# Kernel optimization log

Measured on AMD Instinct MI355X. Metric: run time of the kernel, lower is better.

The kernel has to match this reference:

```python
import jax, jax.numpy as jnp
import numpy as np

D = 2048   # dec_hidden_size == enc_hidden_size
IN = 512   # input_size
T = 4096   # T_enc


def setup_inputs() -> dict:
    key = jax.random.key(0)
    ks = jax.random.split(key, 20)
    s = 0.02
    zeros = jnp.zeros
    return {
        "data": jax.random.normal(ks[0], (1, IN), jnp.float32),
        "h0": jax.random.normal(ks[1], (1, 1, D), jnp.float32),
        "c0": jax.random.normal(ks[2], (1, 1, D), jnp.float32),
        "enc_output": jax.random.normal(ks[3], (T, 1, D), jnp.float32),
        "pi": jax.random.normal(ks[4], (T,), jnp.float32),
        "W_w": jax.random.normal(ks[5], (D, D), jnp.float32) * s,
        "U_w": jax.random.normal(ks[6], (D, D), jnp.float32) * s,
        "V_w": jax.random.normal(ks[7], (1, D), jnp.float32) * s,
        "lin_w": jax.random.normal(ks[8], (D, D), jnp.float32) * s,
        "lin_b": zeros((D,), jnp.float32),
        "lin1_w": jax.random.normal(ks[9], (D, D), jnp.float32) * s,
        "lin1_b": zeros((D,), jnp.float32),
        "lin2_w": jax.random.normal(ks[10], (D, D), jnp.float32) * s,
        "lin2_b": zeros((D,), jnp.float32),
        "dense_w": jax.random.normal(ks[11], (1, D), jnp.float32) * s,
        "dense_b": zeros((1,), jnp.float32),
        "W_ih": jax.random.normal(ks[12], (4 * D, IN + D), jnp.float32) * s,
        "W_hh": jax.random.normal(ks[13], (4 * D, D), jnp.float32) * s,
        "b_ih": zeros((4 * D,), jnp.float32),
        "b_hh": zeros((4 * D,), jnp.float32),
        "i": 100,
    }


def reference(data, h0, c0, enc_output, pi, W_w, U_w, V_w, lin_w, lin_b,
              lin1_w, lin1_b, lin2_w, lin2_b, dense_w, dense_b,
              W_ih, W_hh, b_ih, b_hh, i):
    Tl = pi.shape[0]
    output_pos = i + 1
    enc = enc_output[:, 0, :]                      # (T, E)
    # binary_vector(output_pos, T) @ pi : row k gets pi[output_pos+T-k-2] iff k >= output_pos-1
    k = jnp.arange(Tl)
    idx = output_pos + Tl - k - 2
    prod = jnp.where(k >= output_pos - 1, pi[jnp.clip(idx, 0, Tl - 1)], 0.0)
    u_h = (enc @ U_w.T) * prod[:, None]            # (T, D), per-channel scale by prod
    q = h0[0, 0] @ W_w.T                           # (D,)
    score = jnp.tanh(q[None, :] + u_h) @ V_w[0]    # (T,)
    score = jnp.where(k < output_pos, 0.0, score)  # attn_score[:j_null] = 0 (zero, not -inf)
    attn = jax.nn.softmax(score)                   # softmax over T
    context = attn @ enc                           # (E,)
    x = jnp.concatenate([context, data[0]])        # (E + IN,)
    # single-step LSTM, PyTorch gate order i,f,g,o
    gates = x @ W_ih.T + b_ih + h0[0, 0] @ W_hh.T + b_hh
    gi, gf, gg, go = jnp.split(gates, 4)
    c_new = jax.nn.sigmoid(gf) * c0[0, 0] + jax.nn.sigmoid(gi) * jnp.tanh(gg)
    h_new = jax.nn.sigmoid(go) * jnp.tanh(c_new)
    fc = h_new @ lin_w.T + lin_b
    l1 = fc @ lin1_w.T + lin1_b
    delta = jax.nn.softmax(l1)
    beta = jax.nn.softplus(fc @ lin2_w.T + lin2_b)
    gamma = l1 @ dense_w.T + dense_b               # original reuses linear1 for lin3
    return (gamma, beta, delta, h_new, c_new)
```

## Files before the change

### kernel.cpp

```cpp
#include <hip/hip_runtime.h>
#include <hip/hip_bf16.h>

#define D_  2048
#define IN_ 512
#define T_  4096
#define G4_ 8192

typedef __attribute__((ext_vector_type(4))) float f32x4;
typedef __attribute__((ext_vector_type(8))) short s16x8;
typedef unsigned short u16;

#define WS_PROD    0
#define WS_Q       (T_)
#define WS_X       (T_ + D_)
#define WS_PARTIAL (WS_X + D_ + IN_)
#define WS_ATTN    (WS_PARTIAL + T_*16)
#define WS_GATES   (WS_ATTN + T_)
#define WS_G2      (WS_GATES + G4_)
#define WS_FC      (WS_G2 + G4_)
#define WS_L1      (WS_FC + D_)
#define WS_HN      (WS_L1 + D_)
#define WS_BF16    (WS_HN + D_)
#define WS_FAST_BYTES ((size_t)WS_BF16 * 4 + ((size_t)T_ * D_ + (size_t)D_ * D_) * 2)

typedef const __attribute__((address_space(1))) void gas_t;
typedef __attribute__((address_space(3))) void las_t;

__device__ inline u16 bfbits(float f) {
  union { __hip_bfloat16 b; u16 s; } u; u.b = __float2bfloat16(f); return u.s;
}
__device__ inline float bf2f(u16 s) {
  union { unsigned u; float f; } v; v.u = ((unsigned)s) << 16; return v.f;
}

__device__ inline float wave_dot4(const float* __restrict__ w,
                                  const float* __restrict__ x, int n4, int lane) {
  float s = 0.f;
  const f32x4* w4 = (const f32x4*)w;
  const f32x4* x4 = (const f32x4*)x;
  for (int c = lane; c < n4; c += 64) {
    f32x4 a = w4[c], b = x4[c];
    s += a[0]*b[0] + a[1]*b[1] + a[2]*b[2] + a[3]*b[3];
  }
  #pragma unroll
  for (int m = 32; m >= 1; m >>= 1) s += __shfl_xor(s, m, 64);
  return s;
}

__global__ __launch_bounds__(256) void k_convert(const float* __restrict__ Ww,
    const float* __restrict__ h0, const float* __restrict__ pi,
    const float* __restrict__ data, const int* __restrict__ ip,
    const float* __restrict__ enc, const float* __restrict__ Uw,
    int do_convert, float* __restrict__ ws) {
  const int gidx = blockIdx.x * 256 + threadIdx.x;
  const int nth = 1024 * 256;
  if (do_convert) {
    u16* encB = (u16*)(ws + WS_BF16);
    u16* UwB  = encB + (size_t)T_ * D_;
    for (int c = gidx; c < (T_ * D_) / 8; c += nth) {
      const size_t base = (size_t)c * 8;
      f32x4 v0 = *(const f32x4*)(enc + base);
      f32x4 v1 = *(const f32x4*)(enc + base + 4);
      u16 t[8];
      #pragma unroll
      for (int e = 0; e < 4; ++e) { t[e] = bfbits(v0[e]); t[4 + e] = bfbits(v1[e]); }
      *(s16x8*)&encB[base] = *(s16x8*)&t[0];
    }
    for (int c = gidx; c < (D_ * D_) / 8; c += nth) {
      const size_t base = (size_t)c * 8;
      f32x4 v0 = *(const f32x4*)(Uw + base);
      f32x4 v1 = *(const f32x4*)(Uw + base + 4);
      u16 t[8];
      #pragma unroll
      for (int e = 0; e < 4; ++e) { t[e] = bfbits(v0[e]); t[4 + e] = bfbits(v1[e]); }
      *(s16x8*)&UwB[base] = *(s16x8*)&t[0];
    }
  }
  const int op = ip[0] + 1;
  if (gidx < T_) {
    float p = 0.f;
    if (gidx >= op - 1) {
      int idx = op + T_ - gidx - 2;
      idx = idx < 0 ? 0 : (idx > T_ - 1 ? T_ - 1 : idx);
      p = pi[idx];
    }
    ws[WS_PROD + gidx] = p;
  }
  if (gidx < D_) ws[WS_X + gidx] = 0.f;
  if (gidx < IN_) ws[WS_X + D_ + gidx] = data[gidx];
  const int gw = gidx >> 6, lane = gidx & 63;
  if (gw < D_) {
    float s = wave_dot4(Ww + (size_t)gw * D_, h0, D_ / 4, lane);
    if (lane == 0) ws[WS_Q + gw] = s;
  }
}

__global__ __launch_bounds__(512, 4) void k_gemm_bf16(
    const float* __restrict__ Vw, const float* __restrict__ h0,
    const float* __restrict__ Whh, float* __restrict__ ws) {
  __shared__ __align__(16) u16 Ah[128 * 64];
  __shared__ __align__(16) u16 Bh[128 * 64];
  const u16* encB = (const u16*)(ws + WS_BF16);
  const u16* UwB  = encB + (size_t)T_ * D_;
  const int tid = threadIdx.x, lane = tid & 63, wid = tid >> 6;
  const int wr = wid >> 2, wc = wid & 3;
  const int g = lane >> 4, lr = lane & 15;
  const int bid = blockIdx.x;
  const int wgid = (bid & 7) * 64 + (bid >> 3);
  const int mb = wgid >> 4, nb = wgid & 15;

  f32x4 acc[4][2];
  #pragma unroll
  for (int m = 0; m < 4; ++m)
    #pragma unroll
    for (int n = 0; n < 2; ++n) acc[m][n] = (f32x4){0.f, 0.f, 0.f, 0.f};

  const int c0 = tid,        r0 = c0 >> 3, s0 = (c0 & 7) ^ (r0 & 7);
  const int c1 = tid + 512,  r1 = c1 >> 3, s1 = (c1 & 7) ^ (r1 & 7);
  const u16* ga0 = encB + (size_t)(mb * 128 + r0) * D_ + s0 * 8;
  const u16* ga1 = encB + (size_t)(mb * 128 + r1) * D_ + s1 * 8;
  const u16* gb0 = UwB  + (size_t)(nb * 128 + r0) * D_ + s0 * 8;
  const u16* gb1 = UwB  + (size_t)(nb * 128 + r1) * D_ + s1 * 8;
  u16* la0 = &Ah[c0 * 8]; u16* la1 = &Ah[c1 * 8];
  u16* lb0 = &Bh[c0 * 8]; u16* lb1 = &Bh[c1 * 8];

  for (int ks = 0; ks < D_ / 64; ++ks) {
    __syncthreads();
    __builtin_amdgcn_global_load_lds((gas_t*)(ga0 + ks * 64), (las_t*)la0, 16, 0, 0);
    __builtin_amdgcn_global_load_lds((gas_t*)(ga1 + ks * 64), (las_t*)la1, 16, 0, 0);
    __builtin_amdgcn_global_load_lds((gas_t*)(gb0 + ks * 64), (las_t*)lb0, 16, 0, 0);
    __builtin_amdgcn_global_load_lds((gas_t*)(gb1 + ks * 64), (las_t*)lb1, 16, 0, 0);
    __syncthreads();
    #pragma unroll
    for (int kk = 0; kk < 2; ++kk) {
      const int koff = kk * 64 + g * 16;
      s16x8 af[4], bf[2];
      #pragma unroll
      for (int m = 0; m < 4; ++m) {
        const int r = wr * 64 + m * 16 + lr;
        af[m] = *(const s16x8*)((const char*)Ah + r * 128 + (koff ^ ((r & 7) << 4)));
      }
      #pragma unroll
      for (int n = 0; n < 2; ++n) {
        const int r = wc * 32 + n * 16 + lr;
        bf[n] = *(const s16x8*)((const char*)Bh + r * 128 + (koff ^ ((r & 7) << 4)));
      }
      #pragma unroll
      for (int m = 0; m < 4; ++m)
        #pragma unroll
        for (int n = 0; n < 2; ++n)
          acc[m][n] = __builtin_amdgcn_mfma_f32_16x16x32_bf16(af[m], bf[n], acc[m][n], 0, 0, 0);
    }
  }

  const float* q    = ws + WS_Q;
  const float* prod = ws + WS_PROD;
  float Vv[2], qv[2];
  #pragma unroll
  for (int n = 0; n < 2; ++n) {
    const int d = nb * 128 + wc * 32 + n * 16 + lr;
    Vv[n] = Vw[d]; qv[n] = q[d];
  }
  __syncthreads();
  float* red = (float*)Ah;
  #pragma unroll
  for (int m = 0; m < 4; ++m) {
    #pragma unroll
    for (int r = 0; r < 4; ++r) {
      const int t_loc = wr * 64 + m * 16 + g * 4 + r;
      const float p = prod[mb * 128 + t_loc];
      float s = Vv[0] * tanhf(qv[0] + p * acc[m][0][r])
              + Vv[1] * tanhf(qv[1] + p * acc[m][1][r]);
      s += __shfl_xor(s, 1, 64);
      s += __shfl_xor(s, 2, 64);
      s += __shfl_xor(s, 4, 64);
      s += __shfl_xor(s, 8, 64);
      if (lr == 0) red[t_loc * 4 + wc] = s;
    }
  }
  __syncthreads();
  if (tid < 128) {
    const float s = red[tid * 4] + red[tid * 4 + 1] + red[tid * 4 + 2] + red[tid * 4 + 3];
    ws[WS_PARTIAL + (size_t)(mb * 128 + tid) * 16 + nb] = s;
  }

  const int rbase = bid * 16 + wid * 2;
  #pragma unroll
  for (int rr = 0; rr < 2; ++rr) {
    const int row = rbase + rr;
    float s = wave_dot4(Whh + (size_t)row * D_, h0, D_ / 4, lane);
    if (lane == 0) ws[WS_G2 + row] = s;
  }
}

__global__ __launch_bounds__(512, 4) void k_gemm_f32(
    const float* __restrict__ enc, const float* __restrict__ Uw,
    const float* __restrict__ Vw, const float* __restrict__ h0,
    const float* __restrict__ Whh, float* __restrict__ ws) {
  __shared__ __align__(16) u16 sbuf[2 * 128 * 40];
  u16* Ah = sbuf;
  u16* Bh = sbuf + 128 * 40;
  const int tid = threadIdx.x;
  const int lane = tid & 63, wid = tid >> 6;
  const int wr = wid >> 2, wc = wid & 3;
  const int g = lane >> 4, lr = lane & 15;
  const int mb = blockIdx.x, nb = blockIdx.y;

  f32x4 acc[4][2];
  #pragma unroll
  for (int m = 0; m < 4; ++m)
    #pragma unroll
    for (int n = 0; n < 2; ++n) acc[m][n] = (f32x4){0.f, 0.f, 0.f, 0.f};

  const int srow = tid >> 2;
  const int scol = (tid & 3) * 8;
  const float* pa0 = enc + (size_t)(mb * 128 + srow) * D_ + scol;
  const float* pb0 = Uw  + (size_t)(nb * 128 + srow) * D_ + scol;
  const int sidx = srow * 40 + scol;

  f32x4 an0 = *(const f32x4*)(pa0);
  f32x4 an1 = *(const f32x4*)(pa0 + 4);
  f32x4 bn0 = *(const f32x4*)(pb0);
  f32x4 bn1 = *(const f32x4*)(pb0 + 4);

  for (int ks = 0; ks < 64; ++ks) {
    f32x4 a0 = an0, a1 = an1, b0 = bn0, b1 = bn1;
    if (ks < 63) {
      an0 = *(const f32x4*)(pa0 + (ks + 1) * 32);
      an1 = *(const f32x4*)(pa0 + (ks + 1) * 32 + 4);
      bn0 = *(const f32x4*)(pb0 + (ks + 1) * 32);
      bn1 = *(const f32x4*)(pb0 + (ks + 1) * 32 + 4);
    }
    __syncthreads();
    __align__(16) u16 ah[8], bh[8];
    #pragma unroll
    for (int e = 0; e < 4; ++e) {
      ah[e] = bfbits(a0[e]); ah[4 + e] = bfbits(a1[e]);
      bh[e] = bfbits(b0[e]); bh[4 + e] = bfbits(b1[e]);
    }
    *(s16x8*)&Ah[sidx] = *(s16x8*)&ah[0];
    *(s16x8*)&Bh[sidx] = *(s16x8*)&bh[0];
    __syncthreads();

    s16x8 af[4], bf[2];
    #pragma unroll
    for (int m = 0; m < 4; ++m)
      af[m] = *(const s16x8*)&Ah[(wr * 64 + m * 16 + lr) * 40 + g * 8];
    #pragma unroll
    for (int n = 0; n < 2; ++n)
      bf[n] = *(const s16x8*)&Bh[(wc * 32 + n * 16 + lr) * 40 + g * 8];
    #pragma unroll
    for (int m = 0; m < 4; ++m)
      #pragma unroll
      for (int n = 0; n < 2; ++n)
        acc[m][n] = __builtin_amdgcn_mfma_f32_16x16x32_bf16(af[m], bf[n], acc[m][n], 0, 0, 0);
  }

  const float* q    = ws + WS_Q;
  const float* prod = ws + WS_PROD;
  float Vv[2], qv[2];
  #pragma unroll
  for (int n = 0; n < 2; ++n) {
    const int d = nb * 128 + wc * 32 + n * 16 + lr;
    Vv[n] = Vw[d]; qv[n] = q[d];
  }
  __syncthreads();
  float* red = (float*)sbuf;
  #pragma unroll
  for (int m = 0; m < 4; ++m) {
    #pragma unroll
    for (int r = 0; r < 4; ++r) {
      const int t_loc = wr * 64 + m * 16 + g * 4 + r;
      const float p = prod[mb * 128 + t_loc];
      float s = Vv[0] * tanhf(qv[0] + p * acc[m][0][r])
              + Vv[1] * tanhf(qv[1] + p * acc[m][1][r]);
      s += __shfl_xor(s, 1, 64);
      s += __shfl_xor(s, 2, 64);
      s += __shfl_xor(s, 4, 64);
      s += __shfl_xor(s, 8, 64);
      if (lr == 0) red[t_loc * 4 + wc] = s;
    }
  }
  __syncthreads();
  if (tid < 128) {
    const float s = red[tid * 4] + red[tid * 4 + 1] + red[tid * 4 + 2] + red[tid * 4 + 3];
    ws[WS_PARTIAL + (size_t)(mb * 128 + tid) * 16 + nb] = s;
  }
  const int flat = blockIdx.y * gridDim.x + blockIdx.x;
  const int rbase = flat * 16 + wid * 2;
  #pragma unroll
  for (int rr = 0; rr < 2; ++rr) {
    const int row = rbase + rr;
    float s = wave_dot4(Whh + (size_t)row * D_, h0, D_ / 4, lane);
    if (lane == 0) ws[WS_G2 + row] = s;
  }
}

__global__ __launch_bounds__(1024) void k_attn(const int* __restrict__ ip,
                                               float* __restrict__ ws) {
  __shared__ float sm[16];
  const int tid = threadIdx.x, lane = tid & 63, wid = tid >> 6;
  const int op = ip[0] + 1;
  float v[4];
  #pragma unroll
  for (int j = 0; j < 4; ++j) {
    const int t = tid + j * 1024;
    const f32x4* p = (const f32x4*)(ws + WS_PARTIAL + (size_t)t * 16);
    f32x4 p0 = p[0], p1 = p[1], p2 = p[2], p3 = p[3];
    float s = (p0[0]+p0[1]+p0[2]+p0[3]) + (p1[0]+p1[1]+p1[2]+p1[3])
            + (p2[0]+p2[1]+p2[2]+p2[3]) + (p3[0]+p3[1]+p3[2]+p3[3]);
    v[j] = (t < op) ? 0.f : s;
  }
  float mx = fmaxf(fmaxf(v[0], v[1]), fmaxf(v[2], v[3]));
  #pragma unroll
  for (int m = 32; m >= 1; m >>= 1) mx = fmaxf(mx, __shfl_xor(mx, m, 64));
  if (lane == 0) sm[wid] = mx;
  __syncthreads();
  if (tid == 0) {
    float m2 = sm[0];
    for (int w = 1; w < 16; ++w) m2 = fmaxf(m2, sm[w]);
    sm[0] = m2;
  }
  __syncthreads();
  mx = sm[0];
  __syncthreads();
  float e[4], ls = 0.f;
  #pragma unroll
  for (int j = 0; j < 4; ++j) { e[j] = expf(v[j] - mx); ls += e[j]; }
  #pragma unroll
  for (int m = 32; m >= 1; m >>= 1) ls += __shfl_xor(ls, m, 64);
  if (lane == 0) sm[wid] = ls;
  __syncthreads();
  if (tid == 0) {
    float s2 = 0.f;
    for (int w = 0; w < 16; ++w) s2 += sm[w];
    sm[0] = s2;
  }
  __syncthreads();
  const float inv = 1.f / sm[0];
  #pragma unroll
  for (int j = 0; j < 4; ++j) ws[WS_ATTN + tid + j * 1024] = e[j] * inv;
}

__global__ __launch_bounds__(256) void k_context_bf16(float* __restrict__ ws) {
  const u16* encB = (const u16*)(ws + WS_BF16);
  const int d = blockIdx.x * 256 + threadIdx.x;
  const int t0 = blockIdx.y * 256;
  const float* attn = ws + WS_ATTN;
  float s = 0.f;
  for (int t = t0; t < t0 + 256; ++t) s += attn[t] * bf2f(encB[(size_t)t * D_ + d]);
  atomicAdd(&ws[WS_X + d], s);
}
__global__ __launch_bounds__(256) void k_context_f32(const float* __restrict__ enc,
                                                     float* __restrict__ ws) {
  const int d = blockIdx.x * 256 + threadIdx.x;
  const int t0 = blockIdx.y * 256;
  const float* attn = ws + WS_ATTN;
  float s = 0.f;
  for (int t = t0; t < t0 + 256; ++t) s += attn[t] * enc[(size_t)t * D_ + d];
  atomicAdd(&ws[WS_X + d], s);
}

__global__ __launch_bounds__(256) void k_gatecell(const float* __restrict__ Wih,
    const float* __restrict__ bih, const float* __restrict__ bhh,
    const float* __restrict__ c0, float* __restrict__ ws, float* __restrict__ out) {
  const int wid = threadIdx.x >> 6, lane = threadIdx.x & 63;
  const int d = blockIdx.x * 4 + wid;
  const f32x4* x4 = (const f32x4*)(ws + WS_X);
  const f32x4* r0 = (const f32x4*)(Wih + (size_t)(0 * D_ + d) * (D_ + IN_));
  const f32x4* r1 = (const f32x4*)(Wih + (size_t)(1 * D_ + d) * (D_ + IN_));
  const f32x4* r2 = (const f32x4*)(Wih + (size_t)(2 * D_ + d) * (D_ + IN_));
  const f32x4* r3 = (const f32x4*)(Wih + (size_t)(3 * D_ + d) * (D_ + IN_));
  float s0 = 0.f, s1 = 0.f, s2 = 0.f, s3 = 0.f;
  for (int c = lane; c < (D_ + IN_) / 4; c += 64) {
    f32x4 x = x4[c];
    f32x4 a0 = r0[c], a1 = r1[c], a2 = r2[c], a3 = r3[c];
    s0 += a0[0]*x[0] + a0[1]*x[1] + a0[2]*x[2] + a0[3]*x[3];
    s1 += a1[0]*x[0] + a1[1]*x[1] + a1[2]*x[2] + a1[3]*x[3];
    s2 += a2[0]*x[0] + a2[1]*x[1] + a2[2]*x[2] + a2[3]*x[3];
    s3 += a3[0]*x[0] + a3[1]*x[1] + a3[2]*x[2] + a3[3]*x[3];
  }
  #pragma unroll
  for (int m = 32; m >= 1; m >>= 1) {
    s0 += __shfl_xor(s0, m, 64);
    s1 += __shfl_xor(s1, m, 64);
    s2 += __shfl_xor(s2, m, 64);
    s3 += __shfl_xor(s3, m, 64);
  }
  if (lane == 0) {
    const float gi = s0 + ws[WS_G2 + 0 * D_ + d] + bih[0 * D_ + d] + bhh[0 * D_ + d];
    const float gf = s1 + ws[WS_G2 + 1 * D_ + d] + bih[1 * D_ + d] + bhh[1 * D_ + d];
    const float gg = s2 + ws[WS_G2 + 2 * D_ + d] + bih[2 * D_ + d] + bhh[2 * D_ + d];
    const float go = s3 + ws[WS_G2 + 3 * D_ + d] + bih[3 * D_ + d] + bhh[3 * D_ + d];
    const float si = 1.f / (1.f + expf(-gi));
    const float sf = 1.f / (1.f + expf(-gf));
    const float so = 1.f / (1.f + expf(-go));
    const float cn = sf * c0[d] + si * tanhf(gg);
    const float hn = so * tanhf(cn);
    out[1 + 2 * D_ + d] = hn;
    out[1 + 3 * D_ + d] = cn;
    ws[WS_HN + d] = hn;
  }
}

__global__ __launch_bounds__(256) void k_fc(const float* __restrict__ lw,
    const float* __restrict__ lb, float* __restrict__ ws) {
  const int wid = threadIdx.x >> 6, lane = threadIdx.x & 63;
  const int row = blockIdx.x * 4 + wid;
  float s = wave_dot4(lw + (size_t)row * D_, ws + WS_HN, D_ / 4, lane);
  if (lane == 0) ws[WS_FC + row] = s + lb[row];
}

__global__ __launch_bounds__(256) void k_l1beta(const float* __restrict__ l1w,
    const float* __restrict__ l1b, const float* __restrict__ l2w,
    const float* __restrict__ l2b, float* __restrict__ ws, float* __restrict__ out) {
  const int wid = threadIdx.x >> 6, lane = threadIdx.x & 63;
  const int row = blockIdx.x * 4 + wid;
  float a = wave_dot4(l1w + (size_t)row * D_, ws + WS_FC, D_ / 4, lane);
  float b = wave_dot4(l2w + (size_t)row * D_, ws + WS_FC, D_ / 4, lane);
  if (lane == 0) {
    ws[WS_L1 + row] = a + l1b[row];
    const float x = b + l2b[row];
    out[1 + row] = (x > 20.f) ? x : log1pf(expf(x));
  }
}

__global__ __launch_bounds__(256) void k_final(const float* __restrict__ dw,
    const float* __restrict__ db, float* __restrict__ ws, float* __restrict__ out) {
  __shared__ float sm[4];
  const int tid = threadIdx.x, lane = tid & 63, wid = tid >> 6;
  float v[8];
  #pragma unroll
  for (int j = 0; j < 8; ++j) v[j] = ws[WS_L1 + tid + j * 256];
  float mx = v[0];
  #pragma unroll
  for (int j = 1; j < 8; ++j) mx = fmaxf(mx, v[j]);
  #pragma unroll
  for (int m = 32; m >= 1; m >>= 1) mx = fmaxf(mx, __shfl_xor(mx, m, 64));
  if (lane == 0) sm[wid] = mx;
  __syncthreads();
  mx = fmaxf(fmaxf(sm[0], sm[1]), fmaxf(sm[2], sm[3]));
  __syncthreads();
  float e[8], ls = 0.f;
  #pragma unroll
  for (int j = 0; j < 8; ++j) { e[j] = expf(v[j] - mx); ls += e[j]; }
  #pragma unroll
  for (int m = 32; m >= 1; m >>= 1) ls += __shfl_xor(ls, m, 64);
  if (lane == 0) sm[wid] = ls;
  __syncthreads();
  ls = sm[0] + sm[1] + sm[2] + sm[3];
  __syncthreads();
  const float inv = 1.f / ls;
  float gp = 0.f;
  #pragma unroll
  for (int j = 0; j < 8; ++j) {
    out[1 + D_ + tid + j * 256] = e[j] * inv;
    gp += v[j] * dw[tid + j * 256];
  }
  #pragma unroll
  for (int m = 32; m >= 1; m >>= 1) gp += __shfl_xor(gp, m, 64);
  if (lane == 0) sm[wid] = gp;
  __syncthreads();
  if (tid == 0) out[0] = sm[0] + sm[1] + sm[2] + sm[3] + db[0];
}

extern "C" void kernel_launch(void* const* d_in, const int* in_sizes, int n_in,
                              void* d_out, int out_size, void* d_ws, size_t ws_size,
                              hipStream_t stream) {
  (void)in_sizes; (void)n_in; (void)out_size;
  const float* data   = (const float*)d_in[0];
  const float* h0     = (const float*)d_in[1];
  const float* c0     = (const float*)d_in[2];
  const float* enc    = (const float*)d_in[3];
  const float* pi     = (const float*)d_in[4];
  const float* Ww     = (const float*)d_in[5];
  const float* Uw     = (const float*)d_in[6];
  const float* Vw     = (const float*)d_in[7];
  const float* lin_w  = (const float*)d_in[8];
  const float* lin_b  = (const float*)d_in[9];
  const float* lin1_w = (const float*)d_in[10];
  const float* lin1_b = (const float*)d_in[11];
  const float* lin2_w = (const float*)d_in[12];
  const float* lin2_b = (const float*)d_in[13];
  const float* dw     = (const float*)d_in[14];
  const float* db     = (const float*)d_in[15];
  const float* Wih    = (const float*)d_in[16];
  const float* Whh    = (const float*)d_in[17];
  const float* bih    = (const float*)d_in[18];
  const float* bhh    = (const float*)d_in[19];
  const int*   ip     = (const int*)d_in[20];
  float* ws  = (float*)d_ws;
  float* out = (float*)d_out;
  const int fast = (ws_size >= WS_FAST_BYTES) ? 1 : 0;

  k_convert<<<1024, 256, 0, stream>>>(Ww, h0, pi, data, ip, enc, Uw, fast, ws);
  if (fast)
    k_gemm_bf16<<<512, 512, 0, stream>>>(Vw, h0, Whh, ws);
  else
    k_gemm_f32<<<dim3(T_ / 128, D_ / 128), 512, 0, stream>>>(enc, Uw, Vw, h0, Whh, ws);
  k_attn<<<1, 1024, 0, stream>>>(ip, ws);
  if (fast)
    k_context_bf16<<<dim3(D_ / 256, T_ / 256), 256, 0, stream>>>(ws);
  else
    k_context_f32<<<dim3(D_ / 256, T_ / 256), 256, 0, stream>>>(enc, ws);
  k_gatecell<<<512, 256, 0, stream>>>(Wih, bih, bhh, c0, ws, out);
  k_fc<<<D_ / 4, 256, 0, stream>>>(lin_w, lin_b, ws);
  k_l1beta<<<D_ / 4, 256, 0, stream>>>(lin1_w, lin1_b, lin2_w, lin2_b, ws, out);
  k_final<<<1, 256, 0, stream>>>(dw, db, ws, out);
}
```

Before: 132.6 us.

## Double GEMM K-tile to 128 and move data-part of W_ih matvec into GEMM kernel

The bf16 GEMM now stages 128-wide K slices in LDS with a 16-way XOR swizzle, which halves the number of barrier-separated load/compute iterations. Launch bounds drop to 2 waves-per-EU occupancy because LDS use doubles. Separately, the input-data part of the W_ih product (the last 512 columns) is computed in the GEMM kernel's tail alongside the W_hh matvec, so the gate-cell kernel only handles the context columns. This relies on WS_X+D_ holding data already, which k_convert writes beforehand.

```diff
diff --git a/kernel.cpp b/kernel.cpp
--- a/kernel.cpp
+++ b/kernel.cpp
@@ -95,11 +95,12 @@
   }
 }
 
-__global__ __launch_bounds__(512, 4) void k_gemm_bf16(
+__global__ __launch_bounds__(512, 2) void k_gemm_bf16(
     const float* __restrict__ Vw, const float* __restrict__ h0,
-    const float* __restrict__ Whh, float* __restrict__ ws) {
-  __shared__ __align__(16) u16 Ah[128 * 64];
-  __shared__ __align__(16) u16 Bh[128 * 64];
+    const float* __restrict__ Whh, const float* __restrict__ Wih,
+    float* __restrict__ ws) {
+  __shared__ __align__(16) u16 Ah[128 * 128];
+  __shared__ __align__(16) u16 Bh[128 * 128];
   const u16* encB = (const u16*)(ws + WS_BF16);
   const u16* UwB  = encB + (size_t)T_ * D_;
   const int tid = threadIdx.x, lane = tid & 63, wid = tid >> 6;
@@ -115,35 +116,39 @@
     #pragma unroll
     for (int n = 0; n < 2; ++n) acc[m][n] = (f32x4){0.f, 0.f, 0.f, 0.f};
 
-  const int c0 = tid,        r0 = c0 >> 3, s0 = (c0 & 7) ^ (r0 & 7);
-  const int c1 = tid + 512,  r1 = c1 >> 3, s1 = (c1 & 7) ^ (r1 & 7);
-  const u16* ga0 = encB + (size_t)(mb * 128 + r0) * D_ + s0 * 8;
-  const u16* ga1 = encB + (size_t)(mb * 128 + r1) * D_ + s1 * 8;
-  const u16* gb0 = UwB  + (size_t)(nb * 128 + r0) * D_ + s0 * 8;
-  const u16* gb1 = UwB  + (size_t)(nb * 128 + r1) * D_ + s1 * 8;
-  u16* la0 = &Ah[c0 * 8]; u16* la1 = &Ah[c1 * 8];
-  u16* lb0 = &Bh[c0 * 8]; u16* lb1 = &Bh[c1 * 8];
-
-  for (int ks = 0; ks < D_ / 64; ++ks) {
+  const u16* gA[4]; const u16* gB[4]; int lo[4];
+  #pragma unroll
+  for (int j = 0; j < 4; ++j) {
+    const int c = tid + j * 512;
+    const int r = c >> 4;
+    const int sl = c & 15;
+    const int ss = sl ^ (r & 15);
+    gA[j] = encB + (size_t)(mb * 128 + r) * D_ + ss * 8;
+    gB[j] = UwB  + (size_t)(nb * 128 + r) * D_ + ss * 8;
+    lo[j] = c * 8;
+  }
+
+  for (int ks = 0; ks < D_ / 128; ++ks) {
     __syncthreads();
-    __builtin_amdgcn_global_load_lds((gas_t*)(ga0 + ks * 64), (las_t*)la0, 16, 0, 0);
-    __builtin_amdgcn_global_load_lds((gas_t*)(ga1 + ks * 64), (las_t*)la1, 16, 0, 0);
-    __builtin_amdgcn_global_load_lds((gas_t*)(gb0 + ks * 64), (las_t*)lb0, 16, 0, 0);
-    __builtin_amdgcn_global_load_lds((gas_t*)(gb1 + ks * 64), (las_t*)lb1, 16, 0, 0);
+    #pragma unroll
+    for (int j = 0; j < 4; ++j) {
+      __builtin_amdgcn_global_load_lds((gas_t*)(gA[j] + ks * 128), (las_t*)&Ah[lo[j]], 16, 0, 0);
+      __builtin_amdgcn_global_load_lds((gas_t*)(gB[j] + ks * 128), (las_t*)&Bh[lo[j]], 16, 0, 0);
+    }
     __syncthreads();
     #pragma unroll
-    for (int kk = 0; kk < 2; ++kk) {
-      const int koff = kk * 64 + g * 16;
+    for (int kk = 0; kk < 4; ++kk) {
+      const int sg = kk * 4 + g;
       s16x8 af[4], bf[2];
       #pragma unroll
       for (int m = 0; m < 4; ++m) {
         const int r = wr * 64 + m * 16 + lr;
-        af[m] = *(const s16x8*)((const char*)Ah + r * 128 + (koff ^ ((r & 7) << 4)));
+        af[m] = *(const s16x8*)((const char*)Ah + r * 256 + ((sg ^ (r & 15)) << 4));
       }
       #pragma unroll
       for (int n = 0; n < 2; ++n) {
         const int r = wc * 32 + n * 16 + lr;
-        bf[n] = *(const s16x8*)((const char*)Bh + r * 128 + (koff ^ ((r & 7) << 4)));
+        bf[n] = *(const s16x8*)((const char*)Bh + r * 256 + ((sg ^ (r & 15)) << 4));
       }
       #pragma unroll
       for (int m = 0; m < 4; ++m)
@@ -188,7 +193,8 @@
   #pragma unroll
   for (int rr = 0; rr < 2; ++rr) {
     const int row = rbase + rr;
-    float s = wave_dot4(Whh + (size_t)row * D_, h0, D_ / 4, lane);
+    float s = wave_dot4(Whh + (size_t)row * D_, h0, D_ / 4, lane)
+            + wave_dot4(Wih + (size_t)row * (D_ + IN_) + D_, ws + WS_X + D_, IN_ / 4, lane);
     if (lane == 0) ws[WS_G2 + row] = s;
   }
 }
@@ -196,7 +202,8 @@
 __global__ __launch_bounds__(512, 4) void k_gemm_f32(
     const float* __restrict__ enc, const float* __restrict__ Uw,
     const float* __restrict__ Vw, const float* __restrict__ h0,
-    const float* __restrict__ Whh, float* __restrict__ ws) {
+    const float* __restrict__ Whh, const float* __restrict__ Wih,
+    float* __restrict__ ws) {
   __shared__ __align__(16) u16 sbuf[2 * 128 * 40];
   u16* Ah = sbuf;
   u16* Bh = sbuf + 128 * 40;
@@ -291,7 +298,8 @@
   #pragma unroll
   for (int rr = 0; rr < 2; ++rr) {
     const int row = rbase + rr;
-    float s = wave_dot4(Whh + (size_t)row * D_, h0, D_ / 4, lane);
+    float s = wave_dot4(Whh + (size_t)row * D_, h0, D_ / 4, lane)
+            + wave_dot4(Wih + (size_t)row * (D_ + IN_) + D_, ws + WS_X + D_, IN_ / 4, lane);
     if (lane == 0) ws[WS_G2 + row] = s;
   }
 }
@@ -372,7 +380,7 @@
   const f32x4* r2 = (const f32x4*)(Wih + (size_t)(2 * D_ + d) * (D_ + IN_));
   const f32x4* r3 = (const f32x4*)(Wih + (size_t)(3 * D_ + d) * (D_ + IN_));
   float s0 = 0.f, s1 = 0.f, s2 = 0.f, s3 = 0.f;
-  for (int c = lane; c < (D_ + IN_) / 4; c += 64) {
+  for (int c = lane; c < D_ / 4; c += 64) {
     f32x4 x = x4[c];
     f32x4 a0 = r0[c], a1 = r1[c], a2 = r2[c], a3 = r3[c];
     s0 += a0[0]*x[0] + a0[1]*x[1] + a0[2]*x[2] + a0[3]*x[3];
@@ -495,9 +503,9 @@
 
   k_convert<<<1024, 256, 0, stream>>>(Ww, h0, pi, data, ip, enc, Uw, fast, ws);
   if (fast)
-    k_gemm_bf16<<<512, 512, 0, stream>>>(Vw, h0, Whh, ws);
+    k_gemm_bf16<<<512, 512, 0, stream>>>(Vw, h0, Whh, Wih, ws);
   else
-    k_gemm_f32<<<dim3(T_ / 128, D_ / 128), 512, 0, stream>>>(enc, Uw, Vw, h0, Whh, ws);
+    k_gemm_f32<<<dim3(T_ / 128, D_ / 128), 512, 0, stream>>>(enc, Uw, Vw, h0, Whh, Wih, ws);
   k_attn<<<1, 1024, 0, stream>>>(ip, ws);
   if (fast)
     k_context_bf16<<<dim3(D_ / 256, T_ / 256), 256, 0, stream>>>(ws);
```

After: 132.4 us. Within noise of the previous version (-0.2%).

## Fuse softmax into context kernel and move data-part of W_ih GEMV into gemm

Applied to the files above, without the earlier changes.

The single-block softmax kernel is replaced by a parallel score-reduction kernel. Each context block now recomputes the softmax max and sum redundantly from the 4096 scores and normalizes its own 256 attention weights in shared memory. Separately, the W_ih columns that multiply the input data are folded into the gemm kernel's W_hh GEMV tail, so the gate kernel only streams the context part of W_ih. This removes a serialized 1-block launch and shortens the gate kernel, at the cost of redundant softmax reductions in every context block.

```diff
diff --git a/kernel.cpp b/kernel.cpp
--- a/kernel.cpp
+++ b/kernel.cpp
@@ -14,8 +14,8 @@
 #define WS_Q       (T_)
 #define WS_X       (T_ + D_)
 #define WS_PARTIAL (WS_X + D_ + IN_)
-#define WS_ATTN    (WS_PARTIAL + T_*16)
-#define WS_GATES   (WS_ATTN + T_)
+#define WS_SCORE   (WS_PARTIAL + T_*16)
+#define WS_GATES   (WS_SCORE + T_)
 #define WS_G2      (WS_GATES + G4_)
 #define WS_FC      (WS_G2 + G4_)
 #define WS_L1      (WS_FC + D_)
@@ -97,7 +97,8 @@
 
 __global__ __launch_bounds__(512, 4) void k_gemm_bf16(
     const float* __restrict__ Vw, const float* __restrict__ h0,
-    const float* __restrict__ Whh, float* __restrict__ ws) {
+    const float* __restrict__ Whh, const float* __restrict__ Wih,
+    float* __restrict__ ws) {
   __shared__ __align__(16) u16 Ah[128 * 64];
   __shared__ __align__(16) u16 Bh[128 * 64];
   const u16* encB = (const u16*)(ws + WS_BF16);
@@ -188,7 +189,8 @@
   #pragma unroll
   for (int rr = 0; rr < 2; ++rr) {
     const int row = rbase + rr;
-    float s = wave_dot4(Whh + (size_t)row * D_, h0, D_ / 4, lane);
+    float s = wave_dot4(Whh + (size_t)row * D_, h0, D_ / 4, lane)
+            + wave_dot4(Wih + (size_t)row * (D_ + IN_) + D_, ws + WS_X + D_, IN_ / 4, lane);
     if (lane == 0) ws[WS_G2 + row] = s;
   }
 }
@@ -196,7 +198,8 @@
 __global__ __launch_bounds__(512, 4) void k_gemm_f32(
     const float* __restrict__ enc, const float* __restrict__ Uw,
     const float* __restrict__ Vw, const float* __restrict__ h0,
-    const float* __restrict__ Whh, float* __restrict__ ws) {
+    const float* __restrict__ Whh, const float* __restrict__ Wih,
+    float* __restrict__ ws) {
   __shared__ __align__(16) u16 sbuf[2 * 128 * 40];
   u16* Ah = sbuf;
   u16* Bh = sbuf + 128 * 40;
@@ -291,73 +294,89 @@
   #pragma unroll
   for (int rr = 0; rr < 2; ++rr) {
     const int row = rbase + rr;
-    float s = wave_dot4(Whh + (size_t)row * D_, h0, D_ / 4, lane);
+    float s = wave_dot4(Whh + (size_t)row * D_, h0, D_ / 4, lane)
+            + wave_dot4(Wih + (size_t)row * (D_ + IN_) + D_, ws + WS_X + D_, IN_ / 4, lane);
     if (lane == 0) ws[WS_G2 + row] = s;
   }
 }
 
-__global__ __launch_bounds__(1024) void k_attn(const int* __restrict__ ip,
+__global__ __launch_bounds__(256) void k_score(const int* __restrict__ ip,
                                                float* __restrict__ ws) {
-  __shared__ float sm[16];
+  const int t = blockIdx.x * 256 + threadIdx.x;
+  const int op = ip[0] + 1;
+  const f32x4* p = (const f32x4*)(ws + WS_PARTIAL + (size_t)t * 16);
+  f32x4 p0 = p[0], p1 = p[1], p2 = p[2], p3 = p[3];
+  float s = (p0[0]+p0[1]+p0[2]+p0[3]) + (p1[0]+p1[1]+p1[2]+p1[3])
+          + (p2[0]+p2[1]+p2[2]+p2[3]) + (p3[0]+p3[1]+p3[2]+p3[3]);
+  ws[WS_SCORE + t] = (t < op) ? 0.f : s;
+}
+
+__global__ __launch_bounds__(256) void k_ctxattn_bf16(float* __restrict__ ws) {
+  __shared__ float sred[4];
+  __shared__ float satt[256];
+  const u16* encB = (const u16*)(ws + WS_BF16);
   const int tid = threadIdx.x, lane = tid & 63, wid = tid >> 6;
-  const int op = ip[0] + 1;
-  float v[4];
-  #pragma unroll
-  for (int j = 0; j < 4; ++j) {
-    const int t = tid + j * 1024;
-    const f32x4* p = (const f32x4*)(ws + WS_PARTIAL + (size_t)t * 16);
-    f32x4 p0 = p[0], p1 = p[1], p2 = p[2], p3 = p[3];
-    float s = (p0[0]+p0[1]+p0[2]+p0[3]) + (p1[0]+p1[1]+p1[2]+p1[3])
-            + (p2[0]+p2[1]+p2[2]+p2[3]) + (p3[0]+p3[1]+p3[2]+p3[3]);
-    v[j] = (t < op) ? 0.f : s;
-  }
-  float mx = fmaxf(fmaxf(v[0], v[1]), fmaxf(v[2], v[3]));
+  const float* score = ws + WS_SCORE;
+  float lv[16];
+  #pragma unroll
+  for (int j = 0; j < 16; ++j) lv[j] = score[tid + j * 256];
+  float mx = lv[0];
+  #pragma unroll
+  for (int j = 1; j < 16; ++j) mx = fmaxf(mx, lv[j]);
   #pragma unroll
   for (int m = 32; m >= 1; m >>= 1) mx = fmaxf(mx, __shfl_xor(mx, m, 64));
-  if (lane == 0) sm[wid] = mx;
-  __syncthreads();
-  if (tid == 0) {
-    float m2 = sm[0];
-    for (int w = 1; w < 16; ++w) m2 = fmaxf(m2, sm[w]);
-    sm[0] = m2;
-  }
-  __syncthreads();
-  mx = sm[0];
-  __syncthreads();
-  float e[4], ls = 0.f;
-  #pragma unroll
-  for (int j = 0; j < 4; ++j) { e[j] = expf(v[j] - mx); ls += e[j]; }
+  if (lane == 0) sred[wid] = mx;
+  __syncthreads();
+  mx = fmaxf(fmaxf(sred[0], sred[1]), fmaxf(sred[2], sred[3]));
+  __syncthreads();
+  float ls = 0.f;
+  #pragma unroll
+  for (int j = 0; j < 16; ++j) ls += expf(lv[j] - mx);
   #pragma unroll
   for (int m = 32; m >= 1; m >>= 1) ls += __shfl_xor(ls, m, 64);
-  if (lane == 0) sm[wid] = ls;
-  __syncthreads();
-  if (tid == 0) {
-    float s2 = 0.f;
-    for (int w = 0; w < 16; ++w) s2 += sm[w];
-    sm[0] = s2;
-  }
-  __syncthreads();
-  const float inv = 1.f / sm[0];
-  #pragma unroll
-  for (int j = 0; j < 4; ++j) ws[WS_ATTN + tid + j * 1024] = e[j] * inv;
-}
-
-__global__ __launch_bounds__(256) void k_context_bf16(float* __restrict__ ws) {
-  const u16* encB = (const u16*)(ws + WS_BF16);
+  if (lane == 0) sred[wid] = ls;
+  __syncthreads();
+  const float inv = 1.f / (sred[0] + sred[1] + sred[2] + sred[3]);
+  const int t0 = blockIdx.y * 256;
+  satt[tid] = expf(score[t0 + tid] - mx) * inv;
+  __syncthreads();
   const int d = blockIdx.x * 256 + threadIdx.x;
+  float s = 0.f;
+  for (int t = 0; t < 256; ++t) s += satt[t] * bf2f(encB[(size_t)(t0 + t) * D_ + d]);
+  atomicAdd(&ws[WS_X + d], s);
+}
+__global__ __launch_bounds__(256) void k_ctxattn_f32(const float* __restrict__ enc,
+                                                     float* __restrict__ ws) {
+  __shared__ float sred[4];
+  __shared__ float satt[256];
+  const int tid = threadIdx.x, lane = tid & 63, wid = tid >> 6;
+  const float* score = ws + WS_SCORE;
+  float lv[16];
+  #pragma unroll
+  for (int j = 0; j < 16; ++j) lv[j] = score[tid + j * 256];
+  float mx = lv[0];
+  #pragma unroll
+  for (int j = 1; j < 16; ++j) mx = fmaxf(mx, lv[j]);
+  #pragma unroll
+  for (int m = 32; m >= 1; m >>= 1) mx = fmaxf(mx, __shfl_xor(mx, m, 64));
+  if (lane == 0) sred[wid] = mx;
+  __syncthreads();
+  mx = fmaxf(fmaxf(sred[0], sred[1]), fmaxf(sred[2], sred[3]));
+  __syncthreads();
+  float ls = 0.f;
+  #pragma unroll
+  for (int j = 0; j < 16; ++j) ls += expf(lv[j] - mx);
+  #pragma unroll
+  for (int m = 32; m >= 1; m >>= 1) ls += __shfl_xor(ls, m, 64);
+  if (lane == 0) sred[wid] = ls;
+  __syncthreads();
+  const float inv = 1.f / (sred[0] + sred[1] + sred[2] + sred[3]);
   const int t0 = blockIdx.y * 256;
-  const float* attn = ws + WS_ATTN;
+  satt[tid] = expf(score[t0 + tid] - mx) * inv;
+  __syncthreads();
+  const int d = blockIdx.x * 256 + threadIdx.x;
   float s = 0.f;
-  for (int t = t0; t < t0 + 256; ++t) s += attn[t] * bf2f(encB[(size_t)t * D_ + d]);
-  atomicAdd(&ws[WS_X + d], s);
-}
-__global__ __launch_bounds__(256) void k_context_f32(const float* __restrict__ enc,
-                                                     float* __restrict__ ws) {
-  const int d = blockIdx.x * 256 + threadIdx.x;
-  const int t0 = blockIdx.y * 256;
-  const float* attn = ws + WS_ATTN;
-  float s = 0.f;
-  for (int t = t0; t < t0 + 256; ++t) s += attn[t] * enc[(size_t)t * D_ + d];
+  for (int t = 0; t < 256; ++t) s += satt[t] * enc[(size_t)(t0 + t) * D_ + d];
   atomicAdd(&ws[WS_X + d], s);
 }
 
@@ -372,7 +391,7 @@
   const f32x4* r2 = (const f32x4*)(Wih + (size_t)(2 * D_ + d) * (D_ + IN_));
   const f32x4* r3 = (const f32x4*)(Wih + (size_t)(3 * D_ + d) * (D_ + IN_));
   float s0 = 0.f, s1 = 0.f, s2 = 0.f, s3 = 0.f;
-  for (int c = lane; c < (D_ + IN_) / 4; c += 64) {
+  for (int c = lane; c < D_ / 4; c += 64) {
     f32x4 x = x4[c];
     f32x4 a0 = r0[c], a1 = r1[c], a2 = r2[c], a3 = r3[c];
     s0 += a0[0]*x[0] + a0[1]*x[1] + a0[2]*x[2] + a0[3]*x[3];
@@ -495,14 +514,14 @@
 
   k_convert<<<1024, 256, 0, stream>>>(Ww, h0, pi, data, ip, enc, Uw, fast, ws);
   if (fast)
-    k_gemm_bf16<<<512, 512, 0, stream>>>(Vw, h0, Whh, ws);
+    k_gemm_bf16<<<512, 512, 0, stream>>>(Vw, h0, Whh, Wih, ws);
   else
-    k_gemm_f32<<<dim3(T_ / 128, D_ / 128), 512, 0, stream>>>(enc, Uw, Vw, h0, Whh, ws);
-  k_attn<<<1, 1024, 0, stream>>>(ip, ws);
+    k_gemm_f32<<<dim3(T_ / 128, D_ / 128), 512, 0, stream>>>(enc, Uw, Vw, h0, Whh, Wih, ws);
+  k_score<<<T_ / 256, 256, 0, stream>>>(ip, ws);
   if (fast)
-    k_context_bf16<<<dim3(D_ / 256, T_ / 256), 256, 0, stream>>>(ws);
+    k_ctxattn_bf16<<<dim3(D_ / 256, T_ / 256), 256, 0, stream>>>(ws);
   else
-    k_context_f32<<<dim3(D_ / 256, T_ / 256), 256, 0, stream>>>(enc, ws);
+    k_ctxattn_f32<<<dim3(D_ / 256, T_ / 256), 256, 0, stream>>>(enc, ws);
   k_gatecell<<<512, 256, 0, stream>>>(Wih, bih, bhh, c0, ws, out);
   k_fc<<<D_ / 4, 256, 0, stream>>>(lin_w, lin_b, ws);
   k_l1beta<<<D_ / 4, 256, 0, stream>>>(lin1_w, lin1_b, lin2_w, lin2_b, ws, out);
```

Result: faster. 128.9 us (-2.8%).
